# Performance work log

Hardware: AMD Instinct MI355X
Metric: run time of the kernel (lower is better)

## Reference

```python
import jax, jax.numpy as jnp
import numpy as np

N = 100000   # nodes
E = 1600000  # edges (before self-loops)
HIDDEN = 256
BN_EPS = 1e-5


def setup_inputs() -> dict:
    key = jax.random.key(0)
    ks = jax.random.split(key, 16)
    def lin(k, i, o):
        return jax.random.normal(k, (i, o), jnp.float32) / np.float32(np.sqrt(i))
    inp = {
        "x": jax.random.normal(ks[0], (N, 21), jnp.float32),
        "edge_index": jax.random.randint(ks[1], (2, E), 0, N),
        # GCNConv weights (stored [in, out]) + biases
        "W1": lin(ks[2], 21, HIDDEN), "b1": jnp.zeros((HIDDEN,), jnp.float32),
        "W2": lin(ks[3], HIDDEN, 112), "b2": jnp.zeros((112,), jnp.float32),
        # dense MLP
        "lin2_w": lin(ks[4], 112, 256), "lin2_b": jnp.zeros((256,), jnp.float32),
        "lin3_w": lin(ks[5], 256, 100), "lin3_b": jnp.zeros((100,), jnp.float32),
        "lin4_w": lin(ks[6], 100, 1),   "lin4_b": jnp.zeros((1,), jnp.float32),
        # batchnorm affine params
        "g1": jnp.ones((112,), jnp.float32), "be1": jnp.zeros((112,), jnp.float32),
        "g2": jnp.ones((256,), jnp.float32), "be2": jnp.zeros((256,), jnp.float32),
        "g3": jnp.ones((100,), jnp.float32), "be3": jnp.zeros((100,), jnp.float32),
    }
    return inp


def _gcn_conv(x, W, b, src, dst, n):
    # PyG GCNConv: h = xW; out_i = sum_j norm_ij * h_j (+ bias), sym-normalized w/ self-loops
    h = x @ W                                              # [N, C]
    deg = jax.ops.segment_sum(jnp.ones(src.shape, h.dtype), dst, num_segments=n)
    dinv = jnp.where(deg > 0, jax.lax.rsqrt(deg), 0.0)
    norm = dinv[src] * dinv[dst]                            # [E']
    out = jax.ops.segment_sum(h[src] * norm[:, None], dst, num_segments=n)
    return out + b


def _bn(x, g, b):
    # train-mode batchnorm: biased batch variance
    m = jnp.mean(x, axis=0)
    v = jnp.mean(jnp.square(x - m), axis=0)
    return (x - m) * jax.lax.rsqrt(v + BN_EPS) * g + b


def reference(x, edge_index, W1, b1, W2, b2, lin2_w, lin2_b, lin3_w, lin3_b,
              lin4_w, lin4_b, g1, be1, g2, be2, g3, be3):
    n = x.shape[0]
    loops = jnp.arange(n, dtype=edge_index.dtype)
    src = jnp.concatenate([edge_index[0], loops])
    dst = jnp.concatenate([edge_index[1], loops])
    h = jax.nn.relu(_gcn_conv(x, W1, b1, src, dst, n))
    h = _gcn_conv(h, W2, b2, src, dst, n)
    h = jax.nn.relu(_bn(h, g1, be1))
    # dropout: identity (eval / deterministic)
    h = jax.nn.relu(_bn(h @ lin2_w + lin2_b, g2, be2))
    h = jax.nn.relu(_bn(h @ lin3_w + lin3_b, g3, be3))
    return h @ lin4_w + lin4_b
```

## Files before the change

### kernel.cpp

```cpp
#include <hip/hip_runtime.h>

#define N_NODES 100000
#define N_EDGES 1600000

typedef _Float16 f16x8 __attribute__((ext_vector_type(8)));
typedef _Float16 f16x4 __attribute__((ext_vector_type(4)));
typedef float fx4 __attribute__((ext_vector_type(4)));

#define NREP 16
#define NBUCK 196
#define CHUNK 8192
#define BCAP 12288

__global__ __launch_bounds__(256) void k_bin(const int* __restrict__ ei,
                                             unsigned* __restrict__ binned,
                                             int* __restrict__ gcount) {
  __shared__ unsigned pr[CHUNK];
  __shared__ unsigned srt[CHUNK];
  __shared__ unsigned char bk[CHUNK];
  __shared__ int hist[256], scanb[256], offs[256], bs[256], gb[256];
  const int t = threadIdx.x;
  const int e0 = blockIdx.x * CHUNK;
  const int n = min(CHUNK, N_EDGES - e0);
  hist[t] = 0;
  __syncthreads();
  for (int i = t; i < n; i += 256) {
    int src = ei[e0 + i], dst = ei[N_EDGES + e0 + i];
    int b = dst >> 9;
    pr[i] = ((unsigned)src << 9) | (unsigned)(dst & 511);
    bk[i] = (unsigned char)b;
    atomicAdd(&hist[b], 1);
  }
  __syncthreads();
  int v = hist[t];
  scanb[t] = v;
  __syncthreads();
  for (int off = 1; off < 256; off <<= 1) {
    int a = (t >= off) ? scanb[t - off] : 0;
    __syncthreads();
    scanb[t] += a;
    __syncthreads();
  }
  offs[t] = scanb[t] - v;
  bs[t] = scanb[t] - v;
  __syncthreads();
  for (int i = t; i < n; i += 256) {
    int b = bk[i];
    int p = atomicAdd(&offs[b], 1);
    srt[p] = pr[i];
  }
  if (t < NBUCK && v > 0) gb[t] = atomicAdd(&gcount[t], v);
  __syncthreads();
  int wave = t >> 6, lane = t & 63;
  for (int b = wave; b < NBUCK; b += 4) {
    int c = hist[b];
    if (c == 0) continue;
    int ls = bs[b], base = gb[b];
    unsigned* dstp = binned + (size_t)b * BCAP + base;
    for (int i = lane; i < c; i += 64) dstp[i] = srt[ls + i];
  }
}

__global__ void k_bscan(const int* __restrict__ gcount, int* __restrict__ gbase) {
  __shared__ int s[256];
  int t = threadIdx.x;
  int v = (t < NBUCK) ? gcount[t] : 0;
  s[t] = v;
  __syncthreads();
  for (int off = 1; off < 256; off <<= 1) {
    int a = (t >= off) ? s[t - off] : 0;
    __syncthreads();
    s[t] += a;
    __syncthreads();
  }
  if (t < NBUCK) gbase[t] = s[t] - v;
}

__global__ __launch_bounds__(256) void k_csr(const unsigned* __restrict__ binned,
                                             const int* __restrict__ gcount,
                                             const int* __restrict__ gbase,
                                             int* __restrict__ rowoff,
                                             int* __restrict__ cnt,
                                             float* __restrict__ dinv,
                                             int* __restrict__ csr) {
  __shared__ int hist[512], offs[512], ps[256];
  __shared__ unsigned srt[BCAP];
  const int b = blockIdx.x, t = threadIdx.x;
  const int n = min(gcount[b], BCAP);
  const int gb0 = gbase[b];
  const unsigned* bp = binned + (size_t)b * BCAP;
  hist[t] = 0;
  hist[t + 256] = 0;
  __syncthreads();
  for (int i = t; i < n; i += 256) atomicAdd(&hist[bp[i] & 511], 1);
  __syncthreads();
  int e0v = hist[2 * t], e1v = hist[2 * t + 1];
  ps[t] = e0v + e1v;
  __syncthreads();
  for (int off = 1; off < 256; off <<= 1) {
    int a = (t >= off) ? ps[t - off] : 0;
    __syncthreads();
    ps[t] += a;
    __syncthreads();
  }
  int excl = ps[t] - (e0v + e1v);
  offs[2 * t] = excl;
  offs[2 * t + 1] = excl + e0v;
  __syncthreads();
#pragma unroll
  for (int u = 0; u < 2; ++u) {
    int j = 2 * t + u;
    int nd = (b << 9) + j;
    if (nd < N_NODES) {
      int c = hist[j];
      cnt[nd] = c;
      dinv[nd] = rsqrtf((float)(c + 1));
      rowoff[nd] = gb0 + offs[j];
    }
  }
  __syncthreads();
  for (int i = t; i < n; i += 256) {
    unsigned p = bp[i];
    int d = p & 511;
    int pos = atomicAdd(&offs[d], 1);
    srt[pos] = p >> 9;
  }
  __syncthreads();
  for (int i = t; i < n; i += 256) csr[gb0 + i] = (int)srt[i];
}

__global__ void k_xpad(const float* __restrict__ x, const float* __restrict__ dinv,
                       float* __restrict__ xs) {
  int idx = blockIdx.x * 256 + threadIdx.x;
  if (idx >= N_NODES * 24) return;
  int r = idx / 24, c = idx - r * 24;
  xs[idx] = (c < 21) ? x[r * 21 + c] * dinv[r] : 0.f;
}

__global__ __launch_bounds__(256) void k_aggx(
    const float4* __restrict__ xs4, const float* __restrict__ dinv,
    const int* __restrict__ rowoff, const int* __restrict__ cnt,
    const int* __restrict__ csr, float4* __restrict__ aggx4) {
  int lane = threadIdx.x & 63, wave = threadIdx.x >> 6;
  int j = lane / 6, c4 = lane - j * 6;
  if (j >= 10) return;
  int i = blockIdx.x * 40 + wave * 10 + j;
  float di = dinv[i];
  int start = rowoff[i], len = cnt[i];
  float4 a0 = xs4[i * 6 + c4];
  float4 a1 = make_float4(0.f, 0.f, 0.f, 0.f);
  int e = 0;
  for (; e + 1 < len; e += 2) {
    int s0 = csr[start + e], s1 = csr[start + e + 1];
    float4 u0 = xs4[s0 * 6 + c4];
    float4 u1 = xs4[s1 * 6 + c4];
    a0.x += u0.x; a0.y += u0.y; a0.z += u0.z; a0.w += u0.w;
    a1.x += u1.x; a1.y += u1.y; a1.z += u1.z; a1.w += u1.w;
  }
  if (e < len) {
    int s0 = csr[start + e];
    float4 u0 = xs4[s0 * 6 + c4];
    a0.x += u0.x; a0.y += u0.y; a0.z += u0.z; a0.w += u0.w;
  }
  float4 r;
  r.x = di * (a0.x + a1.x); r.y = di * (a0.y + a1.y);
  r.z = di * (a0.z + a1.z); r.w = di * (a0.w + a1.w);
  aggx4[i * 6 + c4] = r;
}

__global__ __launch_bounds__(256) void k_gemm1(const float4* __restrict__ aggx4,
                                               const float* __restrict__ W1,
                                               const float* __restrict__ b1,
                                               float* __restrict__ h1) {
  __shared__ float As[32][24];
  int t = threadIdx.x;
  int base = blockIdx.x * 32;
  for (int idx = t; idx < 32 * 6; idx += 256) {
    int m = idx / 6, q = idx - m * 6;
    *(float4*)(&As[m][q * 4]) = aggx4[(base + m) * 6 + q];
  }
  float w[21];
#pragma unroll
  for (int k = 0; k < 21; ++k) w[k] = W1[k * 256 + t];
  float bias = b1[t];
  __syncthreads();
  for (int m = 0; m < 32; ++m) {
    float acc = bias;
#pragma unroll
    for (int k = 0; k < 21; ++k) acc = fmaf(As[m][k], w[k], acc);
    h1[(size_t)(base + m) * 256 + t] = fmaxf(acc, 0.f);
  }
}

template <int K, int KPAD, int NOUT, int NR>
__global__ void k_wsplit(const float* __restrict__ W, _Float16* __restrict__ Wh,
                         _Float16* __restrict__ Wl) {
  int idx = blockIdx.x * 256 + threadIdx.x;
  if (idx >= NR * KPAD) return;
  int n = idx / KPAD, k = idx % KPAD;
  float v = (n < NOUT && k < K) ? W[k * NOUT + n] : 0.f;
  _Float16 h = (_Float16)v;
  Wh[idx] = h;
  Wl[idx] = (_Float16)(v - (float)h);
}

template <int K, int KPAD, int NT, int MT, int WR, int WC, bool BN, bool STATS, bool F16OUT>
__global__ __launch_bounds__(256, 3) void k_mgemm(
    const float* __restrict__ A, const _Float16* __restrict__ Wth,
    const _Float16* __restrict__ Wtl, const float* __restrict__ bias,
    const float* __restrict__ bn_a, const float* __restrict__ bn_c,
    const float* __restrict__ rowscale, void* __restrict__ Cv, int NOUTr,
    float* __restrict__ sums, float* __restrict__ sqs) {
  constexpr int BM = WR * MT * 16;
  constexpr int NR = WC * NT * 16;
  constexpr int BKP = 40;
  constexpr int ABYTES = BM * BKP * 2;
  constexpr int BBYTES = NR * BKP * 2;
  __shared__ __align__(16) char smem[2 * ABYTES + 2 * BBYTES];
  _Float16* Ah = (_Float16*)smem;
  _Float16* Al = (_Float16*)(smem + ABYTES);
  _Float16* Bh = (_Float16*)(smem + 2 * ABYTES);
  _Float16* Bl = (_Float16*)(smem + 2 * ABYTES + BBYTES);
  float* C = (float*)Cv;
  _Float16* C16 = (_Float16*)Cv;

  const int tid = threadIdx.x;
  const int lane = tid & 63, wave = tid >> 6;
  const int wr = wave % WR, wc = wave / WR;
  const int quad = lane >> 4, ln = lane & 15;
  const int rowbase = blockIdx.x * BM;

  fx4 acc[MT][NT];
#pragma unroll
  for (int mt = 0; mt < MT; ++mt)
#pragma unroll
    for (int j = 0; j < NT; ++j) acc[mt][j] = (fx4){0.f, 0.f, 0.f, 0.f};

  for (int kc = 0; kc < KPAD / 32; ++kc) {
    __syncthreads();
    for (int idx = tid; idx < BM * 8; idx += 256) {
      int m = idx >> 3, q = idx & 7;
      int gi = rowbase + m;
      int k = kc * 32 + q * 4;
      float vv[4] = {0.f, 0.f, 0.f, 0.f};
      if (gi < N_NODES && k < K) {
        float4 v = *(const float4*)(A + (size_t)gi * K + k);
        if constexpr (BN) {
          float4 a4 = *(const float4*)(bn_a + k);
          float4 c4 = *(const float4*)(bn_c + k);
          v.x = fmaxf(fmaf(v.x, a4.x, c4.x), 0.f);
          v.y = fmaxf(fmaf(v.y, a4.y, c4.y), 0.f);
          v.z = fmaxf(fmaf(v.z, a4.z, c4.z), 0.f);
          v.w = fmaxf(fmaf(v.w, a4.w, c4.w), 0.f);
        }
        vv[0] = v.x; vv[1] = v.y; vv[2] = v.z; vv[3] = v.w;
      }
      f16x4 hi, lo;
#pragma unroll
      for (int t = 0; t < 4; ++t) {
        _Float16 h = (_Float16)vv[t];
        hi[t] = h;
        lo[t] = (_Float16)(vv[t] - (float)h);
      }
      *(f16x4*)(Ah + m * BKP + q * 4) = hi;
      *(f16x4*)(Al + m * BKP + q * 4) = lo;
    }
    for (int idx = tid; idx < NR * 4; idx += 256) {
      int n = idx >> 2, p = idx & 3;
      int src = n * KPAD + kc * 32 + p * 8;
      *(f16x8*)(Bh + n * BKP + p * 8) = *(const f16x8*)(Wth + src);
      *(f16x8*)(Bl + n * BKP + p * 8) = *(const f16x8*)(Wtl + src);
    }
    __syncthreads();
    f16x8 ah[MT], al[MT];
#pragma unroll
    for (int mt = 0; mt < MT; ++mt) {
      int r = (wr * MT + mt) * 16 + ln;
      ah[mt] = *(const f16x8*)(Ah + r * BKP + quad * 8);
      al[mt] = *(const f16x8*)(Al + r * BKP + quad * 8);
    }
#pragma unroll
    for (int j = 0; j < NT; ++j) {
      int n = (wc * NT + j) * 16 + ln;
      f16x8 bh = *(const f16x8*)(Bh + n * BKP + quad * 8);
      f16x8 bl = *(const f16x8*)(Bl + n * BKP + quad * 8);
#pragma unroll
      for (int mt = 0; mt < MT; ++mt)
        acc[mt][j] = __builtin_amdgcn_mfma_f32_16x16x32_f16(ah[mt], bh, acc[mt][j], 0, 0, 0);
#pragma unroll
      for (int mt = 0; mt < MT; ++mt)
        acc[mt][j] = __builtin_amdgcn_mfma_f32_16x16x32_f16(al[mt], bh, acc[mt][j], 0, 0, 0);
#pragma unroll
      for (int mt = 0; mt < MT; ++mt)
        acc[mt][j] = __builtin_amdgcn_mfma_f32_16x16x32_f16(ah[mt], bl, acc[mt][j], 0, 0, 0);
    }
  }

  float rsv[MT][4];
#pragma unroll
  for (int mt = 0; mt < MT; ++mt)
#pragma unroll
    for (int r = 0; r < 4; ++r) {
      int gi = rowbase + (wr * MT + mt) * 16 + quad * 4 + r;
      rsv[mt][r] = (rowscale != nullptr && gi < N_NODES) ? rowscale[gi] : 1.f;
    }

  float scA[NT], sqA[NT];
#pragma unroll
  for (int j = 0; j < NT; ++j) {
    int col = (wc * NT + j) * 16 + ln;
    float bs = (bias != nullptr && col < NOUTr) ? bias[col] : 0.f;
    float sc = 0.f, sq = 0.f;
#pragma unroll
    for (int mt = 0; mt < MT; ++mt) {
      int rb = rowbase + (wr * MT + mt) * 16 + quad * 4;
#pragma unroll
      for (int r = 0; r < 4; ++r) {
        int gi = rb + r;
        if (gi < N_NODES && col < NOUTr) {
          float v = (acc[mt][j][r] + bs) * rsv[mt][r];
          if constexpr (F16OUT)
            C16[(size_t)gi * NOUTr + col] = (_Float16)v;
          else
            C[(size_t)gi * NOUTr + col] = v;
          sc += v;
          sq = fmaf(v, v, sq);
        }
      }
    }
    scA[j] = sc;
    sqA[j] = sq;
  }
  if constexpr (STATS) {
    float* s_s = (float*)smem;
    float* s_q = s_s + NR;
    __syncthreads();
    for (int c = tid; c < 2 * NR; c += 256) s_s[c] = 0.f;
    __syncthreads();
#pragma unroll
    for (int j = 0; j < NT; ++j) {
      float sc = scA[j], sq = sqA[j];
      sc += __shfl_xor(sc, 16); sq += __shfl_xor(sq, 16);
      sc += __shfl_xor(sc, 32); sq += __shfl_xor(sq, 32);
      if (quad == 0) {
        int c = (wc * NT + j) * 16 + ln;
        atomicAdd(&s_s[c], sc);
        atomicAdd(&s_q[c], sq);
      }
    }
    __syncthreads();
    int rep = (blockIdx.x & (NREP - 1));
    for (int c = tid; c < NR; c += 256) {
      if (c < NOUTr) {
        atomicAdd(&sums[rep * NOUTr + c], s_s[c]);
        atomicAdd(&sqs[rep * NOUTr + c], s_q[c]);
      }
    }
  }
}

__global__ __launch_bounds__(256) void k_agg2(
    const f16x8* __restrict__ t2s8, const float* __restrict__ dinv,
    const int* __restrict__ rowoff, const int* __restrict__ cnt,
    const int* __restrict__ csr, const float* __restrict__ b2,
    float* __restrict__ g2) {
  int lane = threadIdx.x & 63, wave = threadIdx.x >> 6;
  int j = lane / 14, c = lane - j * 14;
  if (j >= 4) return;
  int i = blockIdx.x * 16 + wave * 4 + j;
  float di = dinv[i];
  int start = rowoff[i], len = cnt[i];
  f16x8 u = t2s8[i * 14 + c];
  fx4 a0, a1, b0, b1;
#pragma unroll
  for (int t = 0; t < 4; ++t) { a0[t] = (float)u[t]; b0[t] = (float)u[t + 4]; }
  a1 = (fx4){0.f, 0.f, 0.f, 0.f};
  b1 = (fx4){0.f, 0.f, 0.f, 0.f};
  int e = 0;
  for (; e + 1 < len; e += 2) {
    int s0 = csr[start + e], s1 = csr[start + e + 1];
    f16x8 u0 = t2s8[s0 * 14 + c];
    f16x8 u1 = t2s8[s1 * 14 + c];
#pragma unroll
    for (int t = 0; t < 4; ++t) {
      a0[t] += (float)u0[t]; b0[t] += (float)u0[t + 4];
      a1[t] += (float)u1[t]; b1[t] += (float)u1[t + 4];
    }
  }
  if (e < len) {
    int s0 = csr[start + e];
    f16x8 u0 = t2s8[s0 * 14 + c];
#pragma unroll
    for (int t = 0; t < 4; ++t) { a0[t] += (float)u0[t]; b0[t] += (float)u0[t + 4]; }
  }
  float4 blo = *(const float4*)(b2 + c * 8);
  float4 bhi = *(const float4*)(b2 + c * 8 + 4);
  float4 r0, r1;
  r0.x = fmaf(di, a0[0] + a1[0], blo.x); r0.y = fmaf(di, a0[1] + a1[1], blo.y);
  r0.z = fmaf(di, a0[2] + a1[2], blo.z); r0.w = fmaf(di, a0[3] + a1[3], blo.w);
  r1.x = fmaf(di, b0[0] + b1[0], bhi.x); r1.y = fmaf(di, b0[1] + b1[1], bhi.y);
  r1.z = fmaf(di, b0[2] + b1[2], bhi.z); r1.w = fmaf(di, b0[3] + b1[3], bhi.w);
  *(float4*)(g2 + (size_t)i * 112 + c * 8) = r0;
  *(float4*)(g2 + (size_t)i * 112 + c * 8 + 4) = r1;
}

template <int C>
__global__ void k_colstats(const float* __restrict__ X, float* __restrict__ sums,
                           float* __restrict__ sqs) {
  int c = threadIdx.x;
  if (c >= C) return;
  int chunk = (N_NODES + gridDim.x - 1) / gridDim.x;
  int i0 = blockIdx.x * chunk;
  int i1 = min(N_NODES, i0 + chunk);
  float s = 0.f, q = 0.f;
  for (int i = i0; i < i1; ++i) {
    float v = X[(size_t)i * C + c];
    s += v;
    q = fmaf(v, v, q);
  }
  int rep = (blockIdx.x & (NREP - 1));
  atomicAdd(&sums[rep * C + c], s);
  atomicAdd(&sqs[rep * C + c], q);
}

template <int C>
__global__ void k_bnfinal(const float* __restrict__ sums, const float* __restrict__ sqs,
                          const float* __restrict__ gamma, const float* __restrict__ beta,
                          float* __restrict__ bn_a, float* __restrict__ bn_c) {
  int c = threadIdx.x;
  if (c >= C) return;
  float s = 0.f, q = 0.f;
#pragma unroll
  for (int r = 0; r < NREP; ++r) {
    s += sums[r * C + c];
    q += sqs[r * C + c];
  }
  const float inv_n = 1.0f / (float)N_NODES;
  float mean = s * inv_n;
  float var = fmaxf(q * inv_n - mean * mean, 0.f);
  float rstd = 1.0f / sqrtf(var + 1e-5f);
  float a = gamma[c] * rstd;
  bn_a[c] = a;
  bn_c[c] = beta[c] - mean * a;
}

__global__ void k_final(const float* __restrict__ h4, const float* __restrict__ bn_a,
                        const float* __restrict__ bn_c, const float* __restrict__ w4,
                        const float* __restrict__ b4, float* __restrict__ out) {
  int lane = threadIdx.x & 63;
  int i = blockIdx.x * 4 + (threadIdx.x >> 6);
  float acc = fmaxf(fmaf(h4[(size_t)i * 100 + lane], bn_a[lane], bn_c[lane]), 0.f) * w4[lane];
  if (lane < 36) {
    int k = lane + 64;
    acc += fmaxf(fmaf(h4[(size_t)i * 100 + k], bn_a[k], bn_c[k]), 0.f) * w4[k];
  }
#pragma unroll
  for (int off = 32; off >= 1; off >>= 1) acc += __shfl_down(acc, off);
  if (lane == 0) out[i] = acc + b4[0];
}

extern "C" void kernel_launch(void* const* d_in, const int* in_sizes, int n_in,
                              void* d_out, int out_size, void* d_ws, size_t ws_size,
                              hipStream_t stream) {
  const float* x   = (const float*)d_in[0];
  const int*   ei  = (const int*)d_in[1];
  const float* W1  = (const float*)d_in[2];
  const float* b1  = (const float*)d_in[3];
  const float* W2  = (const float*)d_in[4];
  const float* b2  = (const float*)d_in[5];
  const float* l2w = (const float*)d_in[6];
  const float* l2b = (const float*)d_in[7];
  const float* l3w = (const float*)d_in[8];
  const float* l3b = (const float*)d_in[9];
  const float* l4w = (const float*)d_in[10];
  const float* l4b = (const float*)d_in[11];
  const float* g1  = (const float*)d_in[12];
  const float* be1 = (const float*)d_in[13];
  const float* g2w = (const float*)d_in[14];
  const float* be2 = (const float*)d_in[15];
  const float* g3  = (const float*)d_in[16];
  const float* be3 = (const float*)d_in[17];
  float* out = (float*)d_out;

  char* base = (char*)d_ws;
  size_t off = 0;
  auto alloc = [&](size_t bytes) -> char* {
    char* p = base + off;
    off = (off + bytes + 255) & ~(size_t)255;
    return p;
  };
  int*   cnt    = (int*)alloc((size_t)N_NODES * 4);
  int*   rowoff = (int*)alloc((size_t)N_NODES * 4);
  float* dinv   = (float*)alloc((size_t)N_NODES * 4);
  int*   csr    = (int*)alloc((size_t)N_EDGES * 4);
  unsigned* binned = (unsigned*)alloc((size_t)NBUCK * BCAP * 4);
  int*   gcount = (int*)alloc(NBUCK * 4);
  int*   gbase  = (int*)alloc(NBUCK * 4);
  float* stats  = (float*)alloc((size_t)NREP * 960 * 4);
  float* bnco   = (float*)alloc(960 * 4);
  float* xs     = (float*)alloc((size_t)N_NODES * 24 * 4);
  float* aggx   = (float*)alloc((size_t)N_NODES * 24 * 4);
  float* h1     = (float*)alloc((size_t)N_NODES * 256 * 4);
  _Float16* t2s = (_Float16*)alloc((size_t)N_NODES * 112 * 2);
  float* g2buf  = (float*)alloc((size_t)N_NODES * 112 * 4);
  _Float16* wt2h = (_Float16*)alloc(112 * 256 * 2);
  _Float16* wt2l = (_Float16*)alloc(112 * 256 * 2);
  _Float16* wt3h = (_Float16*)alloc(256 * 128 * 2);
  _Float16* wt3l = (_Float16*)alloc(256 * 128 * 2);
  _Float16* wt4h = (_Float16*)alloc(112 * 256 * 2);
  _Float16* wt4l = (_Float16*)alloc(112 * 256 * 2);
  float* h4 = g2buf;

  float* sums1 = stats;
  float* sqs1  = sums1 + NREP * 112;
  float* sums2 = sqs1 + NREP * 112;
  float* sqs2  = sums2 + NREP * 256;
  float* sums3 = sqs2 + NREP * 256;
  float* sqs3  = sums3 + NREP * 112;
  float* bn_a1 = bnco + 0,   *bn_c1 = bnco + 112;
  float* bn_a2 = bnco + 224, *bn_c2 = bnco + 480;
  float* bn_a3 = bnco + 736, *bn_c3 = bnco + 848;

  hipMemsetAsync(gcount, 0, NBUCK * 4, stream);
  hipMemsetAsync(stats, 0, (size_t)NREP * 960 * 4, stream);

  k_bin<<<NBUCK, 256, 0, stream>>>(ei, binned, gcount);
  k_bscan<<<1, 256, 0, stream>>>(gcount, gbase);
  k_csr<<<NBUCK, 256, 0, stream>>>(binned, gcount, gbase, rowoff, cnt, dinv, csr);

  k_wsplit<256, 256, 112, 112><<<112, 256, 0, stream>>>(W2, wt2h, wt2l);
  k_wsplit<112, 128, 256, 256><<<128, 256, 0, stream>>>(l2w, wt3h, wt3l);
  k_wsplit<256, 256, 100, 112><<<112, 256, 0, stream>>>(l3w, wt4h, wt4l);

  k_xpad<<<(N_NODES * 24 + 255) / 256, 256, 0, stream>>>(x, dinv, xs);
  k_aggx<<<2500, 256, 0, stream>>>((const float4*)xs, dinv, rowoff, cnt, csr,
                                   (float4*)aggx);
  k_gemm1<<<3125, 256, 0, stream>>>((const float4*)aggx, W1, b1, h1);

  k_mgemm<256, 256, 7, 2, 4, 1, false, false, true><<<782, 256, 0, stream>>>(
      h1, wt2h, wt2l, nullptr, nullptr, nullptr, dinv, t2s, 112, nullptr, nullptr);
  k_agg2<<<6250, 256, 0, stream>>>((const f16x8*)t2s, dinv, rowoff, cnt, csr, b2,
                                   g2buf);

  k_colstats<112><<<1600, 128, 0, stream>>>(g2buf, sums1, sqs1);
  k_bnfinal<112><<<1, 128, 0, stream>>>(sums1, sqs1, g1, be1, bn_a1, bn_c1);

  k_mgemm<112, 128, 8, 2, 2, 2, true, true, false><<<1563, 256, 0, stream>>>(
      g2buf, wt3h, wt3l, l2b, bn_a1, bn_c1, nullptr, h1, 256, sums2, sqs2);
  k_bnfinal<256><<<1, 256, 0, stream>>>(sums2, sqs2, g2w, be2, bn_a2, bn_c2);

  k_mgemm<256, 256, 7, 2, 4, 1, true, true, false><<<782, 256, 0, stream>>>(
      h1, wt4h, wt4l, l3b, bn_a2, bn_c2, nullptr, h4, 100, sums3, sqs3);
  k_bnfinal<100><<<1, 128, 0, stream>>>(sums3, sqs3, g3, be3, bn_a3, bn_c3);

  k_final<<<25000, 256, 0, stream>>>(h4, bn_a3, bn_c3, l4w, l4b, out);
}
```

Measured before the change: 503.4 us.

## Store h1 activations in fp16 and drop activation low-part MFMA in gemms

The 256-wide intermediate activations (after gemm1 and after lin2) are now stored as fp16 instead of fp32, which halves their global write and read traffic. The split-precision MFMA scheme keeps only the weight hi/lo split, so the activation low-part product and its shared-memory buffer are removed, cutting MFMA work by a third. The operands are swapped so each lane owns four consecutive output channels of one row, which gives vectorized epilogue stores and a per-channel shuffle reduction for the column statistics. Occupancy hints are raised for the K=256 gemms. The trade-off is that activations are rounded to fp16, so accuracy relative to the fp32 reference drops.

```diff
diff --git a/kernel.cpp b/kernel.cpp
--- a/kernel.cpp
+++ b/kernel.cpp
@@ -5,6 +5,7 @@
 
 typedef _Float16 f16x8 __attribute__((ext_vector_type(8)));
 typedef _Float16 f16x4 __attribute__((ext_vector_type(4)));
+typedef _Float16 f16x2 __attribute__((ext_vector_type(2)));
 typedef float fx4 __attribute__((ext_vector_type(4)));
 
 #define NREP 16
@@ -171,7 +172,7 @@
 __global__ __launch_bounds__(256) void k_gemm1(const float4* __restrict__ aggx4,
                                                const float* __restrict__ W1,
                                                const float* __restrict__ b1,
-                                               float* __restrict__ h1) {
+                                               _Float16* __restrict__ h1) {
   __shared__ float As[32][24];
   int t = threadIdx.x;
   int base = blockIdx.x * 32;
@@ -188,7 +189,7 @@
     float acc = bias;
 #pragma unroll
     for (int k = 0; k < 21; ++k) acc = fmaf(As[m][k], w[k], acc);
-    h1[(size_t)(base + m) * 256 + t] = fmaxf(acc, 0.f);
+    h1[(size_t)(base + m) * 256 + t] = (_Float16)fmaxf(acc, 0.f);
   }
 }
 
@@ -204,9 +205,10 @@
   Wl[idx] = (_Float16)(v - (float)h);
 }
 
-template <int K, int KPAD, int NT, int MT, int WR, int WC, bool BN, bool STATS, bool F16OUT>
-__global__ __launch_bounds__(256, 3) void k_mgemm(
-    const float* __restrict__ A, const _Float16* __restrict__ Wth,
+template <int K, int KPAD, int NT, int MT, int WR, int WC, int MINW,
+          bool BN, bool STATS, bool F16IN, bool F16OUT>
+__global__ __launch_bounds__(256, MINW) void k_mgemm(
+    const void* __restrict__ Av, const _Float16* __restrict__ Wth,
     const _Float16* __restrict__ Wtl, const float* __restrict__ bias,
     const float* __restrict__ bn_a, const float* __restrict__ bn_c,
     const float* __restrict__ rowscale, void* __restrict__ Cv, int NOUTr,
@@ -216,11 +218,12 @@
   constexpr int BKP = 40;
   constexpr int ABYTES = BM * BKP * 2;
   constexpr int BBYTES = NR * BKP * 2;
-  __shared__ __align__(16) char smem[2 * ABYTES + 2 * BBYTES];
+  __shared__ __align__(16) char smem[ABYTES + 2 * BBYTES];
   _Float16* Ah = (_Float16*)smem;
-  _Float16* Al = (_Float16*)(smem + ABYTES);
-  _Float16* Bh = (_Float16*)(smem + 2 * ABYTES);
-  _Float16* Bl = (_Float16*)(smem + 2 * ABYTES + BBYTES);
+  _Float16* Bh = (_Float16*)(smem + ABYTES);
+  _Float16* Bl = (_Float16*)(smem + ABYTES + BBYTES);
+  const float* A32 = (const float*)Av;
+  const _Float16* A16 = (const _Float16*)Av;
   float* C = (float*)Cv;
   _Float16* C16 = (_Float16*)Cv;
 
@@ -238,32 +241,47 @@
 
   for (int kc = 0; kc < KPAD / 32; ++kc) {
     __syncthreads();
-    for (int idx = tid; idx < BM * 8; idx += 256) {
-      int m = idx >> 3, q = idx & 7;
+    for (int idx = tid; idx < BM * 4; idx += 256) {
+      int m = idx >> 2, q = idx & 3;
       int gi = rowbase + m;
-      int k = kc * 32 + q * 4;
-      float vv[4] = {0.f, 0.f, 0.f, 0.f};
+      int k = kc * 32 + q * 8;
+      f16x8 hv;
+#pragma unroll
+      for (int t = 0; t < 8; ++t) hv[t] = (_Float16)0;
       if (gi < N_NODES && k < K) {
-        float4 v = *(const float4*)(A + (size_t)gi * K + k);
-        if constexpr (BN) {
-          float4 a4 = *(const float4*)(bn_a + k);
-          float4 c4 = *(const float4*)(bn_c + k);
-          v.x = fmaxf(fmaf(v.x, a4.x, c4.x), 0.f);
-          v.y = fmaxf(fmaf(v.y, a4.y, c4.y), 0.f);
-          v.z = fmaxf(fmaf(v.z, a4.z, c4.z), 0.f);
-          v.w = fmaxf(fmaf(v.w, a4.w, c4.w), 0.f);
+        if constexpr (F16IN) {
+          hv = *(const f16x8*)(A16 + (size_t)gi * K + k);
+          if constexpr (BN) {
+            float4 a0 = *(const float4*)(bn_a + k);
+            float4 a1 = *(const float4*)(bn_a + k + 4);
+            float4 c0 = *(const float4*)(bn_c + k);
+            float4 c1 = *(const float4*)(bn_c + k + 4);
+            float av[8] = {a0.x, a0.y, a0.z, a0.w, a1.x, a1.y, a1.z, a1.w};
+            float cv[8] = {c0.x, c0.y, c0.z, c0.w, c1.x, c1.y, c1.z, c1.w};
+#pragma unroll
+            for (int t = 0; t < 8; ++t)
+              hv[t] = (_Float16)fmaxf(fmaf((float)hv[t], av[t], cv[t]), 0.f);
+          }
+        } else {
+          float4 v0 = *(const float4*)(A32 + (size_t)gi * K + k);
+          float4 v1 = *(const float4*)(A32 + (size_t)gi * K + k + 4);
+          float vv[8] = {v0.x, v0.y, v0.z, v0.w, v1.x, v1.y, v1.z, v1.w};
+          if constexpr (BN) {
+            float4 a0 = *(const float4*)(bn_a + k);
+            float4 a1 = *(const float4*)(bn_a + k + 4);
+            float4 c0 = *(const float4*)(bn_c + k);
+            float4 c1 = *(const float4*)(bn_c + k + 4);
+            float av[8] = {a0.x, a0.y, a0.z, a0.w, a1.x, a1.y, a1.z, a1.w};
+            float cv[8] = {c0.x, c0.y, c0.z, c0.w, c1.x, c1.y, c1.z, c1.w};
+#pragma unroll
+            for (int t = 0; t < 8; ++t)
+              vv[t] = fmaxf(fmaf(vv[t], av[t], cv[t]), 0.f);
+          }
+#pragma unroll
+          for (int t = 0; t < 8; ++t) hv[t] = (_Float16)vv[t];
         }
-        vv[0] = v.x; vv[1] = v.y; vv[2] = v.z; vv[3] = v.w;
       }
-      f16x4 hi, lo;
-#pragma unroll
-      for (int t = 0; t < 4; ++t) {
-        _Float16 h = (_Float16)vv[t];
-        hi[t] = h;
-        lo[t] = (_Float16)(vv[t] - (float)h);
-      }
-      *(f16x4*)(Ah + m * BKP + q * 4) = hi;
-      *(f16x4*)(Al + m * BKP + q * 4) = lo;
+      *(f16x8*)(Ah + m * BKP + q * 8) = hv;
     }
     for (int idx = tid; idx < NR * 4; idx += 256) {
       int n = idx >> 2, p = idx & 3;
@@ -272,82 +290,87 @@
       *(f16x8*)(Bl + n * BKP + p * 8) = *(const f16x8*)(Wtl + src);
     }
     __syncthreads();
-    f16x8 ah[MT], al[MT];
+    f16x8 nf[MT];
 #pragma unroll
     for (int mt = 0; mt < MT; ++mt) {
       int r = (wr * MT + mt) * 16 + ln;
-      ah[mt] = *(const f16x8*)(Ah + r * BKP + quad * 8);
-      al[mt] = *(const f16x8*)(Al + r * BKP + quad * 8);
+      nf[mt] = *(const f16x8*)(Ah + r * BKP + quad * 8);
     }
 #pragma unroll
     for (int j = 0; j < NT; ++j) {
       int n = (wc * NT + j) * 16 + ln;
-      f16x8 bh = *(const f16x8*)(Bh + n * BKP + quad * 8);
-      f16x8 bl = *(const f16x8*)(Bl + n * BKP + quad * 8);
+      f16x8 wh = *(const f16x8*)(Bh + n * BKP + quad * 8);
+      f16x8 wl = *(const f16x8*)(Bl + n * BKP + quad * 8);
 #pragma unroll
       for (int mt = 0; mt < MT; ++mt)
-        acc[mt][j] = __builtin_amdgcn_mfma_f32_16x16x32_f16(ah[mt], bh, acc[mt][j], 0, 0, 0);
+        acc[mt][j] = __builtin_amdgcn_mfma_f32_16x16x32_f16(wh, nf[mt], acc[mt][j], 0, 0, 0);
 #pragma unroll
       for (int mt = 0; mt < MT; ++mt)
-        acc[mt][j] = __builtin_amdgcn_mfma_f32_16x16x32_f16(al[mt], bh, acc[mt][j], 0, 0, 0);
-#pragma unroll
-      for (int mt = 0; mt < MT; ++mt)
-        acc[mt][j] = __builtin_amdgcn_mfma_f32_16x16x32_f16(ah[mt], bl, acc[mt][j], 0, 0, 0);
-    }
-  }
-
-  float rsv[MT][4];
-#pragma unroll
-  for (int mt = 0; mt < MT; ++mt)
-#pragma unroll
-    for (int r = 0; r < 4; ++r) {
-      int gi = rowbase + (wr * MT + mt) * 16 + quad * 4 + r;
-      rsv[mt][r] = (rowscale != nullptr && gi < N_NODES) ? rowscale[gi] : 1.f;
-    }
-
-  float scA[NT], sqA[NT];
+        acc[mt][j] = __builtin_amdgcn_mfma_f32_16x16x32_f16(wl, nf[mt], acc[mt][j], 0, 0, 0);
+    }
+  }
+
+  float* s_s = (float*)smem;
+  float* s_q = s_s + NR;
+  __syncthreads();
+  if constexpr (STATS) {
+    for (int c = tid; c < 2 * NR; c += 256) s_s[c] = 0.f;
+    __syncthreads();
+  }
+  float rs[MT];
+#pragma unroll
+  for (int mt = 0; mt < MT; ++mt) {
+    int nd = rowbase + (wr * MT + mt) * 16 + ln;
+    rs[mt] = (rowscale != nullptr && nd < N_NODES) ? rowscale[nd] : 1.f;
+  }
 #pragma unroll
   for (int j = 0; j < NT; ++j) {
-    int col = (wc * NT + j) * 16 + ln;
-    float bs = (bias != nullptr && col < NOUTr) ? bias[col] : 0.f;
-    float sc = 0.f, sq = 0.f;
+    int ch0 = (wc * NT + j) * 16 + quad * 4;
+    bool cv = ch0 < NOUTr;
+    float4 b4 = make_float4(0.f, 0.f, 0.f, 0.f);
+    if (cv && bias != nullptr) b4 = *(const float4*)(bias + ch0);
+    float sc[4] = {0.f, 0.f, 0.f, 0.f}, sq[4] = {0.f, 0.f, 0.f, 0.f};
 #pragma unroll
     for (int mt = 0; mt < MT; ++mt) {
-      int rb = rowbase + (wr * MT + mt) * 16 + quad * 4;
-#pragma unroll
-      for (int r = 0; r < 4; ++r) {
-        int gi = rb + r;
-        if (gi < N_NODES && col < NOUTr) {
-          float v = (acc[mt][j][r] + bs) * rsv[mt][r];
-          if constexpr (F16OUT)
-            C16[(size_t)gi * NOUTr + col] = (_Float16)v;
-          else
-            C[(size_t)gi * NOUTr + col] = v;
-          sc += v;
-          sq = fmaf(v, v, sq);
+      int nd = rowbase + (wr * MT + mt) * 16 + ln;
+      if (nd < N_NODES && cv) {
+        float v0 = (acc[mt][j][0] + b4.x) * rs[mt];
+        float v1 = (acc[mt][j][1] + b4.y) * rs[mt];
+        float v2 = (acc[mt][j][2] + b4.z) * rs[mt];
+        float v3 = (acc[mt][j][3] + b4.w) * rs[mt];
+        if constexpr (F16OUT) {
+          f16x4 o = {(_Float16)v0, (_Float16)v1, (_Float16)v2, (_Float16)v3};
+          *(f16x4*)(C16 + (size_t)nd * NOUTr + ch0) = o;
+        } else {
+          float4 o = make_float4(v0, v1, v2, v3);
+          *(float4*)(C + (size_t)nd * NOUTr + ch0) = o;
+        }
+        if constexpr (STATS) {
+          sc[0] += v0; sq[0] = fmaf(v0, v0, sq[0]);
+          sc[1] += v1; sq[1] = fmaf(v1, v1, sq[1]);
+          sc[2] += v2; sq[2] = fmaf(v2, v2, sq[2]);
+          sc[3] += v3; sq[3] = fmaf(v3, v3, sq[3]);
         }
       }
     }
-    scA[j] = sc;
-    sqA[j] = sq;
+    if constexpr (STATS) {
+      if (cv) {
+#pragma unroll
+        for (int r = 0; r < 4; ++r) {
+          float s = sc[r], q = sq[r];
+          s += __shfl_xor(s, 1); q += __shfl_xor(q, 1);
+          s += __shfl_xor(s, 2); q += __shfl_xor(q, 2);
+          s += __shfl_xor(s, 4); q += __shfl_xor(q, 4);
+          s += __shfl_xor(s, 8); q += __shfl_xor(q, 8);
+          if (ln == 0) {
+            atomicAdd(&s_s[ch0 + r], s);
+            atomicAdd(&s_q[ch0 + r], q);
+          }
+        }
+      }
+    }
   }
   if constexpr (STATS) {
-    float* s_s = (float*)smem;
-    float* s_q = s_s + NR;
-    __syncthreads();
-    for (int c = tid; c < 2 * NR; c += 256) s_s[c] = 0.f;
-    __syncthreads();
-#pragma unroll
-    for (int j = 0; j < NT; ++j) {
-      float sc = scA[j], sq = sqA[j];
-      sc += __shfl_xor(sc, 16); sq += __shfl_xor(sq, 16);
-      sc += __shfl_xor(sc, 32); sq += __shfl_xor(sq, 32);
-      if (quad == 0) {
-        int c = (wc * NT + j) * 16 + ln;
-        atomicAdd(&s_s[c], sc);
-        atomicAdd(&s_q[c], sq);
-      }
-    }
     __syncthreads();
     int rep = (blockIdx.x & (NREP - 1));
     for (int c = tid; c < NR; c += 256) {
@@ -500,7 +523,7 @@
   float* bnco   = (float*)alloc(960 * 4);
   float* xs     = (float*)alloc((size_t)N_NODES * 24 * 4);
   float* aggx   = (float*)alloc((size_t)N_NODES * 24 * 4);
-  float* h1     = (float*)alloc((size_t)N_NODES * 256 * 4);
+  _Float16* h1  = (_Float16*)alloc((size_t)N_NODES * 256 * 2);
   _Float16* t2s = (_Float16*)alloc((size_t)N_NODES * 112 * 2);
   float* g2buf  = (float*)alloc((size_t)N_NODES * 112 * 4);
   _Float16* wt2h = (_Float16*)alloc(112 * 256 * 2);
@@ -537,7 +560,7 @@
                                    (float4*)aggx);
   k_gemm1<<<3125, 256, 0, stream>>>((const float4*)aggx, W1, b1, h1);
 
-  k_mgemm<256, 256, 7, 2, 4, 1, false, false, true><<<782, 256, 0, stream>>>(
+  k_mgemm<256, 256, 7, 2, 4, 1, 4, false, false, true, true><<<782, 256, 0, stream>>>(
       h1, wt2h, wt2l, nullptr, nullptr, nullptr, dinv, t2s, 112, nullptr, nullptr);
   k_agg2<<<6250, 256, 0, stream>>>((const f16x8*)t2s, dinv, rowoff, cnt, csr, b2,
                                    g2buf);
@@ -545,11 +568,11 @@
   k_colstats<112><<<1600, 128, 0, stream>>>(g2buf, sums1, sqs1);
   k_bnfinal<112><<<1, 128, 0, stream>>>(sums1, sqs1, g1, be1, bn_a1, bn_c1);
 
-  k_mgemm<112, 128, 8, 2, 2, 2, true, true, false><<<1563, 256, 0, stream>>>(
+  k_mgemm<112, 128, 8, 2, 2, 2, 3, true, true, false, true><<<1563, 256, 0, stream>>>(
       g2buf, wt3h, wt3l, l2b, bn_a1, bn_c1, nullptr, h1, 256, sums2, sqs2);
   k_bnfinal<256><<<1, 256, 0, stream>>>(sums2, sqs2, g2w, be2, bn_a2, bn_c2);
 
-  k_mgemm<256, 256, 7, 2, 4, 1, true, true, false><<<782, 256, 0, stream>>>(
+  k_mgemm<256, 256, 7, 2, 4, 1, 4, true, true, true, false><<<782, 256, 0, stream>>>(
       h1, wt4h, wt4l, l3b, bn_a2, bn_c2, nullptr, h4, 100, sums3, sqs3);
   k_bnfinal<100><<<1, 128, 0, stream>>>(sums3, sqs3, g3, be3, bn_a3, bn_c3);
 
```

After: 467.8 us. 7.1% less time.
